# Performance work log

Hardware: AMD Instinct MI355X
Metric: run time of the kernel (lower is better)

## Reference

```python
import jax, jax.numpy as jnp
import numpy as np

N = 50000       # nodes
E = 1_600_000   # edges (avg degree 32)
IN = 256        # in_dim
HID = 64        # hidden_dim
HEADS = 2
CLS = 10
NEG_SLOPE = 0.2  # PyG GATConv default leaky_relu slope


def gat_layer(x, edge_index, W, att_src, att_dst, bias, heads, concat):
    """PyG-style GATConv (eval mode, add_self_loops=True).
    x: [N, F_in]; W: [F_in, heads*C]; att_src/att_dst: [heads, C]; bias: [heads*C] or [C].
    """
    n = x.shape[0]
    loop = jnp.arange(n)
    src = jnp.concatenate([edge_index[0], loop])   # message sources j
    dst = jnp.concatenate([edge_index[1], loop])   # message targets i
    C = W.shape[1] // heads
    h = (x @ W).reshape(n, heads, C)               # [N, H, C]
    a_s = jnp.sum(h * att_src, axis=-1)            # [N, H]
    a_d = jnp.sum(h * att_dst, axis=-1)            # [N, H]
    e = jax.nn.leaky_relu(a_s[src] + a_d[dst], NEG_SLOPE)   # [E', H]
    # segment softmax over incoming edges of each destination node
    m = jax.lax.stop_gradient(jax.ops.segment_max(e, dst, num_segments=n))
    ex = jnp.exp(e - m[dst])
    denom = jax.ops.segment_sum(ex, dst, num_segments=n)
    alpha = ex / denom[dst]                         # [E', H]
    out = jax.ops.segment_sum(alpha[:, :, None] * h[src], dst, num_segments=n)  # [N, H, C]
    out = out.reshape(n, heads * C) if concat else out.mean(axis=1)
    return out + bias


def setup_inputs() -> dict:
    key = jax.random.key(0)
    ks = jax.random.split(key, 12)
    sd = lambda f: np.float32(1.0 / np.sqrt(f))
    x = jax.random.normal(ks[0], (N, IN), dtype=jnp.float32)
    edge_index = jax.random.randint(ks[1], (2, E), 0, N, dtype=jnp.int64)
    # layer 1: in_dim -> hidden, heads=2, concat
    W1 = jax.random.normal(ks[2], (IN, HEADS * HID), dtype=jnp.float32) * sd(IN)
    as1 = jax.random.normal(ks[3], (HEADS, HID), dtype=jnp.float32) * sd(HID)
    ad1 = jax.random.normal(ks[4], (HEADS, HID), dtype=jnp.float32) * sd(HID)
    b1 = jnp.zeros((HEADS * HID,), dtype=jnp.float32)
    # layer 2: hidden*heads -> hidden, heads=1, concat=False
    W2 = jax.random.normal(ks[5], (HEADS * HID, HID), dtype=jnp.float32) * sd(HEADS * HID)
    as2 = jax.random.normal(ks[6], (1, HID), dtype=jnp.float32) * sd(HID)
    ad2 = jax.random.normal(ks[7], (1, HID), dtype=jnp.float32) * sd(HID)
    b2 = jnp.zeros((HID,), dtype=jnp.float32)
    # linear head
    Wl = jax.random.normal(ks[8], (HID, CLS), dtype=jnp.float32) * sd(HID)
    bl = jnp.zeros((CLS,), dtype=jnp.float32)
    return {"x": x, "edge_index": edge_index,
            "W1": W1, "as1": as1, "ad1": ad1, "b1": b1,
            "W2": W2, "as2": as2, "ad2": ad2, "b2": b2,
            "Wl": Wl, "bl": bl}


def reference(x, edge_index, W1, as1, ad1, b1, W2, as2, ad2, b2, Wl, bl):
    h = jax.nn.elu(gat_layer(x, edge_index, W1, as1, ad1, b1, HEADS, True))
    h = jax.nn.elu(gat_layer(h, edge_index, W2, as2, ad2, b2, 1, False))
    return h @ Wl + bl  # [N, num_classes]
```

## Files before the change

### kernel.cpp

```cpp
#include <hip/hip_runtime.h>

#define NN 50000
#define NE 1600000
#define EP (NE + NN)
#define IN_DIM 256
#define HIDD 64
#define NCLS 10
#define NBKT 196
#define EPB 8192
#define NPB ((EP + EPB - 1) / EPB)
#define BCAP 12288

typedef unsigned short u16;
typedef short bf16x8 __attribute__((ext_vector_type(8)));
typedef float f32x4 __attribute__((ext_vector_type(4)));

__device__ __forceinline__ float b2f(u16 v) { return __uint_as_float(((unsigned)v) << 16); }
__device__ __forceinline__ u16 f2b(float f) {
    unsigned u = __float_as_uint(f);
    unsigned r = (u + 0x7FFFu + ((u >> 16) & 1u)) >> 16;
    return (u16)r;
}

__device__ __forceinline__ void load_edge(const int* __restrict__ ei, int m, int g,
                                          int& s, int& d) {
    if (g < NE) {
        if (m) { s = ei[2 * (size_t)g]; d = ei[2 * ((size_t)NE + g)]; }
        else   { s = ei[g];             d = ei[NE + g]; }
    } else {
        s = d = g - NE;
    }
    s = s < 0 ? 0 : (s >= NN ? NN - 1 : s);
    d = d < 0 ? 0 : (d >= NN ? NN - 1 : d);
}

__device__ __forceinline__ void wcvt_att_job(
    const float* __restrict__ W, const float* __restrict__ as,
    const float* __restrict__ ad, int K, int N, int H, u16* __restrict__ Wt,
    int idx) {
    if (idx >= K * (N + 16)) return;
    int n = idx / K, k = idx - n * K;
    if (n < N) { Wt[idx] = f2b(W[(size_t)k * N + n]); return; }
    int j = n - N;
    if (j >= 2 * H) { Wt[idx] = 0; return; }
    const float* att = (j & 1) ? ad : as;
    int h = j >> 1, C = N / H;
    float sum = 0.f;
    for (int c = 0; c < C; ++c)
        sum += W[(size_t)k * N + h * C + c] * att[h * C + c];
    Wt[idx] = f2b(sum);
}

__global__ __launch_bounds__(1024) void partition_k(
    const int* __restrict__ ei, int* __restrict__ gcursor,
    unsigned* __restrict__ bbuf,
    const float* __restrict__ W1, const float* __restrict__ as1,
    const float* __restrict__ ad1, u16* __restrict__ w1t,
    const float* __restrict__ W2, const float* __restrict__ as2,
    const float* __restrict__ ad2, u16* __restrict__ w2t) {
    __shared__ int hist[NBKT], base[NBKT], cur[NBKT];
    __shared__ unsigned stash[EPB];
    __shared__ int smode;
    int t = threadIdx.x, b = blockIdx.x;
    if (b < 36) wcvt_att_job(W1, as1, ad1, 256, 128, 2, w1t, b * 1024 + t);
    else if (b < 46) wcvt_att_job(W2, as2, ad2, 128, 64, 1, w2t, (b - 36) * 1024 + t);
    if (t < 64) {
        int nz = 0;
#pragma unroll
        for (int k = 0; k < 4; ++k)
            if (ei[2 * (t * 4 + k) + 1] != 0) nz = 1;
        unsigned long long bal = __ballot(nz);
        if (t == 0) smode = (bal == 0ULL) ? 1 : 0;
    }
    for (int i = t; i < NBKT; i += 1024) hist[i] = 0;
    __syncthreads();
    int m = smode;
    int g0 = b * EPB;
    int gend = min(g0 + EPB, EP);
    for (int g = g0 + t; g < gend; g += 1024) {
        int s, d;
        load_edge(ei, m, g, s, d);
        stash[g - g0] = ((unsigned)s << 16) | (unsigned)d;
        atomicAdd(&hist[d >> 8], 1);
    }
    __syncthreads();
    for (int i = t; i < NBKT; i += 1024) {
        base[i] = hist[i] ? atomicAdd(&gcursor[i], hist[i]) : 0;
        cur[i] = 0;
    }
    __syncthreads();
    int cnt = gend - g0;
    for (int l = t; l < cnt; l += 1024) {
        unsigned p = stash[l];
        int d = p & 0xFFFF;
        int bb = d >> 8;
        int r = base[bb] + atomicAdd(&cur[bb], 1);
        if (r < BCAP)
            bbuf[(size_t)bb * BCAP + r] = ((p >> 16) << 8) | (unsigned)(d & 255);
    }
}

__global__ __launch_bounds__(1024) void bucket_csr_k(const unsigned* __restrict__ bbuf,
                                                     const int* __restrict__ gcursor,
                                                     int* __restrict__ row_ptr,
                                                     u16* __restrict__ csr_src) {
    __shared__ int bsc[256];
    __shared__ int hist[256], scn[256], cur[256];
    __shared__ int se0, scnt, stot;
    int b = blockIdx.x, t = threadIdx.x;
    int v = 0;
    if (t < 256) {
        v = (t < NBKT) ? min(gcursor[t], BCAP) : 0;
        bsc[t] = v;
        hist[t] = 0;
    }
    __syncthreads();
    for (int off = 1; off < 256; off <<= 1) {
        int x = (t < 256 && t >= off) ? bsc[t - off] : 0;
        __syncthreads();
        if (t < 256) bsc[t] += x;
        __syncthreads();
    }
    if (t == b) { se0 = bsc[t] - v; scnt = v; }
    if (t == NBKT - 1) stot = bsc[t];
    __syncthreads();
    int e0 = se0, cnt = scnt;
    const unsigned* bb = bbuf + (size_t)b * BCAP;
    for (int e = t; e < cnt; e += 1024)
        atomicAdd(&hist[bb[e] & 255], 1);
    __syncthreads();
    int hv = 0;
    if (t < 256) { hv = hist[t]; scn[t] = hv; }
    __syncthreads();
    for (int off = 1; off < 256; off <<= 1) {
        int x = (t < 256 && t >= off) ? scn[t - off] : 0;
        __syncthreads();
        if (t < 256) scn[t] += x;
        __syncthreads();
    }
    if (t < 256) {
        int ex = scn[t] - hv;
        int n = b * 256 + t;
        if (n < NN) row_ptr[n] = e0 + ex;
        cur[t] = e0 + ex;
    }
    __syncthreads();
    for (int e = t; e < cnt; e += 1024) {
        unsigned p = bb[e];
        int pos = atomicAdd(&cur[p & 255], 1);
        csr_src[pos] = (u16)(p >> 8);
    }
    if (b == 0 && t == 0) row_ptr[NN] = stot;
}

template <int K, int NF, int H, bool F32A>
__global__ __launch_bounds__(256) void gemm_mfma_att_k(
    const float* __restrict__ Af, const u16* __restrict__ Ab,
    const u16* __restrict__ Wt, u16* __restrict__ C,
    float* __restrict__ a_s, float* __restrict__ a_d) {
    constexpr int NTF = NF / 16, NT = NTF + 1, KS = K / 32;
    const int wave = threadIdx.x >> 6, lane = threadIdx.x & 63;
    const int quad = lane >> 4, l15 = lane & 15;
    const int m0 = blockIdx.x * 64 + wave * 16;
    int rowA = m0 + l15;
    if (rowA >= NN) rowA = NN - 1;
    const float* afp = F32A ? (Af + (size_t)rowA * K + quad * 8) : nullptr;
    const u16*   abp = F32A ? nullptr : (Ab + (size_t)rowA * K + quad * 8);
    const u16* bptr = Wt + (size_t)l15 * K + quad * 8;
    f32x4 acc[NT] = {};
#pragma unroll
    for (int ks = 0; ks < KS; ++ks) {
        bf16x8 af;
        if (F32A) {
            float4 v0 = *(const float4*)(afp + ks * 32);
            float4 v1 = *(const float4*)(afp + ks * 32 + 4);
            af[0] = (short)f2b(v0.x); af[1] = (short)f2b(v0.y);
            af[2] = (short)f2b(v0.z); af[3] = (short)f2b(v0.w);
            af[4] = (short)f2b(v1.x); af[5] = (short)f2b(v1.y);
            af[6] = (short)f2b(v1.z); af[7] = (short)f2b(v1.w);
        } else {
            af = *(const bf16x8*)(abp + ks * 32);
        }
        bf16x8 bf[NT];
#pragma unroll
        for (int nt = 0; nt < NT; ++nt)
            bf[nt] = *(const bf16x8*)(bptr + (size_t)nt * 16 * K + ks * 32);
#pragma unroll
        for (int nt = 0; nt < NT; ++nt)
            acc[nt] = __builtin_amdgcn_mfma_f32_16x16x32_bf16(af, bf[nt], acc[nt], 0, 0, 0);
    }
#pragma unroll
    for (int nt = 0; nt < NTF; ++nt) {
#pragma unroll
        for (int reg = 0; reg < 4; ++reg) {
            int row = m0 + quad * 4 + reg;
            if (row < NN) C[(size_t)row * NF + nt * 16 + l15] = f2b(acc[nt][reg]);
        }
    }
    if (l15 < 2 * H) {
        int h = l15 >> 1;
        float* dst = (l15 & 1) ? a_d : a_s;
#pragma unroll
        for (int reg = 0; reg < 4; ++reg) {
            int row = m0 + quad * 4 + reg;
            if (row < NN) dst[row * H + h] = acc[NTF][reg];
        }
    }
}

template <int CH, int H, bool HEAD>
__global__ __launch_bounds__(256) void gat_gather_k(
    const int* __restrict__ row_ptr, const u16* __restrict__ csr_src,
    const float* __restrict__ a_s, const float* __restrict__ a_d,
    const u16* __restrict__ h, const float* __restrict__ bias,
    u16* __restrict__ outg, const float* __restrict__ Wl,
    const float* __restrict__ bl, float* __restrict__ outh) {
    constexpr int VEC = CH / 64;
    constexpr int JB = 16;
    int n = (blockIdx.x * blockDim.x + threadIdx.x) >> 6;
    int lane = threadIdx.x & 63;
    if (n >= NN) return;
    int r0 = row_ptr[n], r1 = row_ptr[n + 1];
    const bool hi = (VEC == 2) ? (lane >= 32) : false;
    const int shl16 = hi ? 0 : 16;

    float adn0, adn1 = 0.f;
    if (H == 2) {
        float2 adv = *(const float2*)(a_d + n * 2);
        adn0 = adv.x; adn1 = adv.y;
    } else {
        adn0 = a_d[n];
    }

    float dh0 = 0.f, dh1 = 0.f;
    float acc[VEC];
#pragma unroll
    for (int v = 0; v < VEC; ++v) acc[v] = 0.f;

    for (int base = r0; base < r1; base += 64) {
        int cnt = min(64, r1 - base);
        int idx = base + lane;
        bool act = idx < r1;
        int sl = act ? (int)csr_src[idx] : 0;
        unsigned pex;
        if (H == 2) {
            float2 av = *(const float2*)(a_s + sl * 2);
            float e0 = av.x + adn0;
            e0 = e0 > 0.f ? e0 : 0.2f * e0;
            e0 = fminf(e0, 60.f);
            float ex0 = act ? __expf(e0) : 0.f;
            dh0 += ex0;
            float e1 = av.y + adn1;
            e1 = e1 > 0.f ? e1 : 0.2f * e1;
            e1 = fminf(e1, 60.f);
            float ex1 = act ? __expf(e1) : 0.f;
            dh1 += ex1;
            pex = (unsigned)f2b(ex0) | ((unsigned)f2b(ex1) << 16);
        } else {
            float e0 = a_s[sl] + adn0;
            e0 = e0 > 0.f ? e0 : 0.2f * e0;
            e0 = fminf(e0, 60.f);
            float ex0 = act ? __expf(e0) : 0.f;
            dh0 += ex0;
            pex = (unsigned)sl | ((unsigned)f2b(ex0) << 16);
        }
        for (int j0 = 0; j0 < cnt; j0 += JB) {
            if (VEC == 2) {
                int ssu[JB];
                unsigned peu[JB];
#pragma unroll
                for (int i = 0; i < JB; ++i) {
                    ssu[i] = __builtin_amdgcn_readlane(sl, j0 + i);
                    peu[i] = (unsigned)__builtin_amdgcn_readlane((int)pex, j0 + i);
                }
                unsigned hv[JB];
#pragma unroll
                for (int i = 0; i < JB; ++i)
                    hv[i] = ((const unsigned*)(h + (size_t)ssu[i] * CH))[lane];
#pragma unroll
                for (int i = 0; i < JB; ++i) {
                    float exv = __uint_as_float((peu[i] << shl16) & 0xFFFF0000u);
                    acc[0] += exv * __uint_as_float(hv[i] << 16);
                    acc[1] += exv * __uint_as_float(hv[i] & 0xFFFF0000u);
                }
            } else {
                unsigned peu[JB];
#pragma unroll
                for (int i = 0; i < JB; ++i)
                    peu[i] = (unsigned)__builtin_amdgcn_readlane((int)pex, j0 + i);
                u16 hv[JB];
#pragma unroll
                for (int i = 0; i < JB; ++i)
                    hv[i] = (h + (size_t)(peu[i] & 0xFFFFu) * CH)[lane];
#pragma unroll
                for (int i = 0; i < JB; ++i)
                    acc[0] += __uint_as_float(peu[i] & 0xFFFF0000u) * b2f(hv[i]);
            }
        }
    }

#pragma unroll
    for (int off = 32; off; off >>= 1) dh0 += __shfl_xor(dh0, off);
    float dn = dh0;
    if (H == 2) {
#pragma unroll
        for (int off = 32; off; off >>= 1) dh1 += __shfl_xor(dh1, off);
        dn = hi ? dh1 : dh0;
    }

    if (VEC == 2) {
        int c = lane * 2;
        float2 bv = *(const float2*)(bias + c);
        float v0 = acc[0] / dn + bv.x;
        float v1 = acc[1] / dn + bv.y;
        v0 = v0 > 0.f ? v0 : expm1f(v0);
        v1 = v1 > 0.f ? v1 : expm1f(v1);
        ushort2 ov;
        ov.x = f2b(v0); ov.y = f2b(v1);
        *(ushort2*)(outg + (size_t)n * CH + c) = ov;
    } else {
        float v0 = acc[0] / dn + bias[lane];
        v0 = v0 > 0.f ? v0 : expm1f(v0);
        if (HEAD) {
#pragma unroll
            for (int cls = 0; cls < NCLS; ++cls) {
                float p = v0 * Wl[lane * NCLS + cls];
#pragma unroll
                for (int off = 32; off; off >>= 1) p += __shfl_xor(p, off);
                if (lane == cls) outh[(size_t)n * NCLS + cls] = p + bl[cls];
            }
        } else {
            outg[(size_t)n * CH + lane] = f2b(v0);
        }
    }
}

extern "C" void kernel_launch(void* const* d_in, const int* in_sizes, int n_in,
                              void* d_out, int out_size, void* d_ws, size_t ws_size,
                              hipStream_t stream) {
    const float* x   = (const float*)d_in[0];
    const int*   ei  = (const int*)d_in[1];
    const float* W1  = (const float*)d_in[2];
    const float* as1 = (const float*)d_in[3];
    const float* ad1 = (const float*)d_in[4];
    const float* b1  = (const float*)d_in[5];
    const float* W2  = (const float*)d_in[6];
    const float* as2 = (const float*)d_in[7];
    const float* ad2 = (const float*)d_in[8];
    const float* b2  = (const float*)d_in[9];
    const float* Wl  = (const float*)d_in[10];
    const float* bl  = (const float*)d_in[11];
    float* out = (float*)d_out;

    float* ws = (float*)d_ws;
    size_t o = 0;
    u16* hb  = (u16*)(ws + o); o += (size_t)NN * 64;
    u16* g1  = (u16*)(ws + o); o += (size_t)NN * 64;
    unsigned* bbuf = (unsigned*)g1;
    u16* w1t = (u16*)(ws + o); o += 144 * 256 / 2;
    u16* w2t = (u16*)(ws + o); o += 80 * 128 / 2;
    float* a_s = ws + o;       o += (size_t)NN * 2;
    float* a_d = ws + o;       o += (size_t)NN * 2;
    int* ints = (int*)(ws + o);
    size_t io = 0;
    int* gcursor  = ints + io; io += NBKT;
    int* row_ptr  = ints + io; io += NN + 1;
    u16* csr_src  = (u16*)(ints + io); io += (EP + 1) / 2;

    hipMemsetAsync(gcursor, 0, NBKT * sizeof(int), stream);
    partition_k<<<NPB, 1024, 0, stream>>>(ei, gcursor, bbuf,
                                          W1, as1, ad1, w1t, W2, as2, ad2, w2t);
    bucket_csr_k<<<NBKT, 1024, 0, stream>>>(bbuf, gcursor, row_ptr, csr_src);

    const int gatherBlocks = (NN + 3) / 4;
    const int gemmBlocks = (NN + 63) / 64;

    gemm_mfma_att_k<256, 128, 2, true><<<gemmBlocks, 256, 0, stream>>>(
        x, nullptr, w1t, hb, a_s, a_d);
    gat_gather_k<128, 2, false><<<gatherBlocks, 256, 0, stream>>>(
        row_ptr, csr_src, a_s, a_d, hb, b1, g1, nullptr, nullptr, nullptr);

    gemm_mfma_att_k<128, 64, 1, false><<<gemmBlocks, 256, 0, stream>>>(
        nullptr, g1, w2t, hb, a_s, a_d);
    gat_gather_k<64, 1, true><<<gatherBlocks, 256, 0, stream>>>(
        row_ptr, csr_src, a_s, a_d, hb, b2, nullptr, Wl, bl, out);
}
```

Before: 312.5 us.

## Gather neighbor features with 16-byte loads split across lane groups

```diff
diff --git a/kernel.cpp b/kernel.cpp
--- a/kernel.cpp
+++ b/kernel.cpp
@@ -14,6 +14,7 @@
 typedef unsigned short u16;
 typedef short bf16x8 __attribute__((ext_vector_type(8)));
 typedef float f32x4 __attribute__((ext_vector_type(4)));
+typedef unsigned u32x4 __attribute__((ext_vector_type(4)));
 
 __device__ __forceinline__ float b2f(u16 v) { return __uint_as_float(((unsigned)v) << 16); }
 __device__ __forceinline__ u16 f2b(float f) {
@@ -215,14 +216,19 @@
     const u16* __restrict__ h, const float* __restrict__ bias,
     u16* __restrict__ outg, const float* __restrict__ Wl,
     const float* __restrict__ bl, float* __restrict__ outh) {
-    constexpr int VEC = CH / 64;
-    constexpr int JB = 16;
+    constexpr int LPR = CH / 8;
+    constexpr int G = 64 / LPR;
+    constexpr int SH = (CH == 128) ? 8 : 7;
     int n = (blockIdx.x * blockDim.x + threadIdx.x) >> 6;
     int lane = threadIdx.x & 63;
     if (n >= NN) return;
     int r0 = row_ptr[n], r1 = row_ptr[n + 1];
-    const bool hi = (VEC == 2) ? (lane >= 32) : false;
-    const int shl16 = hi ? 0 : 16;
+    const int q = lane & (LPR - 1);
+    const int g = lane >> ((CH == 128) ? 4 : 3);
+    const int g4 = g * 4;
+    const unsigned qoff = (unsigned)q * 16u;
+    const int shl16 = (q < LPR / 2) ? 16 : 0;
+    const unsigned char* h8 = (const unsigned char*)h;
 
     float adn0, adn1 = 0.f;
     if (H == 2) {
@@ -233,9 +239,9 @@
     }
 
     float dh0 = 0.f, dh1 = 0.f;
-    float acc[VEC];
-#pragma unroll
-    for (int v = 0; v < VEC; ++v) acc[v] = 0.f;
+    float acc[8];
+#pragma unroll
+    for (int v = 0; v < 8; ++v) acc[v] = 0.f;
 
     for (int base = r0; base < r1; base += 64) {
         int cnt = min(64, r1 - base);
@@ -264,37 +270,33 @@
             dh0 += ex0;
             pex = (unsigned)sl | ((unsigned)f2b(ex0) << 16);
         }
-        for (int j0 = 0; j0 < cnt; j0 += JB) {
-            if (VEC == 2) {
-                int ssu[JB];
-                unsigned peu[JB];
-#pragma unroll
-                for (int i = 0; i < JB; ++i) {
-                    ssu[i] = __builtin_amdgcn_readlane(sl, j0 + i);
-                    peu[i] = (unsigned)__builtin_amdgcn_readlane((int)pex, j0 + i);
+        for (int j0 = 0; j0 < cnt; j0 += 4 * G) {
+            int per[4], slr[4];
+#pragma unroll
+            for (int i = 0; i < 4; ++i) {
+                int a = ((j0 + i * G) << 2) + g4;
+                per[i] = __builtin_amdgcn_ds_bpermute(a, (int)pex);
+                if (H == 2) slr[i] = __builtin_amdgcn_ds_bpermute(a, sl);
+            }
+            u32x4 hv[4];
+#pragma unroll
+            for (int i = 0; i < 4; ++i) {
+                unsigned row = (H == 2) ? (unsigned)slr[i]
+                                        : ((unsigned)per[i] & 0xFFFFu);
+                hv[i] = *(const u32x4*)(h8 + ((row << SH) + qoff));
+            }
+#pragma unroll
+            for (int i = 0; i < 4; ++i) {
+                unsigned ex = (H == 2)
+                    ? ((((unsigned)per[i]) << shl16) & 0xFFFF0000u)
+                    : (((unsigned)per[i]) & 0xFFFF0000u);
+                float exf = __uint_as_float(ex);
+#pragma unroll
+                for (int d = 0; d < 4; ++d) {
+                    unsigned w = hv[i][d];
+                    acc[2 * d]     += exf * __uint_as_float(w << 16);
+                    acc[2 * d + 1] += exf * __uint_as_float(w & 0xFFFF0000u);
                 }
-                unsigned hv[JB];
-#pragma unroll
-                for (int i = 0; i < JB; ++i)
-                    hv[i] = ((const unsigned*)(h + (size_t)ssu[i] * CH))[lane];
-#pragma unroll
-                for (int i = 0; i < JB; ++i) {
-                    float exv = __uint_as_float((peu[i] << shl16) & 0xFFFF0000u);
-                    acc[0] += exv * __uint_as_float(hv[i] << 16);
-                    acc[1] += exv * __uint_as_float(hv[i] & 0xFFFF0000u);
-                }
-            } else {
-                unsigned peu[JB];
-#pragma unroll
-                for (int i = 0; i < JB; ++i)
-                    peu[i] = (unsigned)__builtin_amdgcn_readlane((int)pex, j0 + i);
-                u16 hv[JB];
-#pragma unroll
-                for (int i = 0; i < JB; ++i)
-                    hv[i] = (h + (size_t)(peu[i] & 0xFFFFu) * CH)[lane];
-#pragma unroll
-                for (int i = 0; i < JB; ++i)
-                    acc[0] += __uint_as_float(peu[i] & 0xFFFF0000u) * b2f(hv[i]);
             }
         }
     }
@@ -305,32 +307,49 @@
     if (H == 2) {
 #pragma unroll
         for (int off = 32; off; off >>= 1) dh1 += __shfl_xor(dh1, off);
-        dn = hi ? dh1 : dh0;
-    }
-
-    if (VEC == 2) {
-        int c = lane * 2;
-        float2 bv = *(const float2*)(bias + c);
-        float v0 = acc[0] / dn + bv.x;
-        float v1 = acc[1] / dn + bv.y;
+        dn = (q < LPR / 2) ? dh0 : dh1;
+    }
+#pragma unroll
+    for (int v = 0; v < 8; ++v) {
+#pragma unroll
+        for (int off = LPR; off < 64; off <<= 1)
+            acc[v] += __shfl_xor(acc[v], off);
+    }
+
+    if (HEAD) {
+        float t01 = (lane & 8) ? acc[1] : acc[0];
+        float t23 = (lane & 8) ? acc[3] : acc[2];
+        float t45 = (lane & 8) ? acc[5] : acc[4];
+        float t67 = (lane & 8) ? acc[7] : acc[6];
+        float ta = (lane & 16) ? t23 : t01;
+        float tb = (lane & 16) ? t67 : t45;
+        float ts = (lane & 32) ? tb : ta;
+        int srcl = ((lane & 7) << 3) | (lane >> 3);
+        float vsw = __uint_as_float(
+            __builtin_amdgcn_ds_bpermute(srcl << 2, __float_as_int(ts)));
+        float v0 = vsw / dn + bias[lane];
         v0 = v0 > 0.f ? v0 : expm1f(v0);
-        v1 = v1 > 0.f ? v1 : expm1f(v1);
-        ushort2 ov;
-        ov.x = f2b(v0); ov.y = f2b(v1);
-        *(ushort2*)(outg + (size_t)n * CH + c) = ov;
+#pragma unroll
+        for (int cls = 0; cls < NCLS; ++cls) {
+            float p = v0 * Wl[lane * NCLS + cls];
+#pragma unroll
+            for (int off = 32; off; off >>= 1) p += __shfl_xor(p, off);
+            if (lane == cls) outh[(size_t)n * NCLS + cls] = p + bl[cls];
+        }
     } else {
-        float v0 = acc[0] / dn + bias[lane];
-        v0 = v0 > 0.f ? v0 : expm1f(v0);
-        if (HEAD) {
-#pragma unroll
-            for (int cls = 0; cls < NCLS; ++cls) {
-                float p = v0 * Wl[lane * NCLS + cls];
-#pragma unroll
-                for (int off = 32; off; off >>= 1) p += __shfl_xor(p, off);
-                if (lane == cls) outh[(size_t)n * NCLS + cls] = p + bl[cls];
+        if (g == 0) {
+            float vv[8];
+#pragma unroll
+            for (int k = 0; k < 8; ++k) {
+                float t = acc[k] / dn + bias[q * 8 + k];
+                vv[k] = t > 0.f ? t : expm1f(t);
             }
-        } else {
-            outg[(size_t)n * CH + lane] = f2b(v0);
+            u32x4 ov;
+#pragma unroll
+            for (int d = 0; d < 4; ++d)
+                ov[d] = (unsigned)f2b(vv[2 * d]) |
+                        ((unsigned)f2b(vv[2 * d + 1]) << 16);
+            *(u32x4*)(outg + (size_t)n * CH + q * 8) = ov;
         }
     }
 }
```

After: 315.4 us. About the same (+0.9%).
